# Kernel optimization log

Measured on AMD Instinct MI355X. Metric: run time of the kernel, lower is better.

Reference implementation:

```python
import jax, jax.numpy as jnp
import numpy as np

B = 64        # num_groups
G = 32        # group_size
D = 2000      # output dim (counts per bin/gene)
M = 16        # m_samples
E = 16        # noise_dim
DIN = 256
LAM = 1.0
TRUST = 0.25
SMOOTH = 1e-8
IPF_ITERS = 60
EPS = 1e-12


def _arch(x, noise, W, b):
    # simple linear architecture: concat(x, noise) @ W + b
    return jnp.concatenate([x, noise], axis=-1) @ W + b


def _loss(x, target, W, b, noise_loss):
    # replicate each row m times (unsqueeze(1).expand(...).reshape == repeat)
    x_rep = jnp.repeat(x, M, axis=0)                      # [n*M, DIN]
    pred = _arch(x_rep, noise_loss, W, b)                 # [n*M, D] (no act_fn in loss path)
    pred = pred.reshape(B, G, M, D).sum(axis=1)           # [B, M, D]
    term_conf = jnp.linalg.norm(pred - target[:, None, :], axis=2).mean(axis=1)  # [B]
    sq = jnp.sum(pred * pred, axis=2)                     # [B, M]
    inn = jnp.einsum('bmd,bnd->bmn', pred, pred)          # [B, M, M]
    sqd = jnp.clip(sq[:, :, None] + sq[:, None, :] - 2.0 * inn, 1e-6)
    d = jnp.sqrt(sqd)
    mask = 1.0 - jnp.eye(M, dtype=d.dtype)
    mean_pd = jnp.sum(d * mask, axis=(1, 2)) / (M * (M - 1))
    return jnp.mean(term_conf - (LAM / 2.0) * mean_pd)


def _ipf(x_pred, C):
    # KL/I-projection with row anchoring (keep_rows=True, trust_clip=0.25)
    y = jnp.clip(x_pred, 0.0)
    C = jnp.clip(C.astype(y.dtype), 0.0)
    R = y.sum(axis=2)                                     # [B, G] anchor row totals
    col_zero = (y.sum(axis=1) <= 0) & (C > 0)
    y = y + SMOOTH * col_zero[:, None, :].astype(y.dtype)
    row_zero = (y.sum(axis=2) <= 0) & (R > 0)
    y = y + SMOOTH * row_zero[:, :, None].astype(y.dtype)

    def body(_, y):
        col = jnp.clip(y.sum(axis=1), EPS)
        y = y * jnp.clip(C / col, 1.0 - TRUST, 1.0 + TRUST)[:, None, :]
        row = jnp.clip(y.sum(axis=2), EPS)
        y = y * jnp.clip(R / row, 1.0 - TRUST, 1.0 + TRUST)[:, :, None]
        return y

    y = jax.lax.fori_loop(0, IPF_ITERS, body, y)
    col = jnp.clip(y.sum(axis=1), EPS)
    return y * (C / col)[:, None, :]


def _rank(v, descending):
    # rank along last axis via double argsort (0 = first picked)
    order = jnp.argsort(-v if descending else v, axis=-1)
    return jnp.argsort(order, axis=-1)


def _round_to_targets(x, target_bd):
    # exact integerization across G per (B, D); jit-safe full-G rank replaces dynamic-k topk+scatter
    x = jnp.clip(x, 0.0)
    xf = jnp.floor(x)
    y = xf.astype(jnp.int32)                              # [B, G, D]
    frac = x - xf
    need = target_bd - y.sum(axis=1)                      # [B, D]
    pos = jnp.clip(need, 0)
    q = pos // G
    y = y + q[:, None, :]
    r = pos - q * G
    rank = _rank(jnp.transpose(frac, (0, 2, 1)), descending=True)   # [B, D, G]
    add = (rank < r[:, :, None]).astype(jnp.int32)
    y = y + jnp.transpose(add, (0, 2, 1))
    # negative residuals: remove from smallest frac among y > 0
    need = target_bd - y.sum(axis=1)
    neg = jnp.clip(-need, 0)
    neg = jnp.minimum(neg, y.sum(axis=1))
    q = neg // G
    y_before = y
    y = jnp.clip(y - q[:, None, :], 0)
    removed = (y_before - y).sum(axis=1)
    r = neg - removed
    frac_m = jnp.where(y > 0, frac, jnp.inf)
    rank = _rank(jnp.transpose(frac_m, (0, 2, 1)), descending=False)
    rem = (rank < r[:, :, None]).astype(jnp.int32)
    y = jnp.clip(y - jnp.transpose(rem, (0, 2, 1)), 0)
    return y


def setup_inputs() -> dict:
    key = jax.random.key(0)
    ks = jax.random.split(key, 6)
    x = jax.random.normal(ks[0], (B * G, DIN), dtype=jnp.float32)
    target = jax.random.uniform(ks[1], (B, D), dtype=jnp.float32) * 100.0
    target_sum = jax.random.randint(ks[2], (B, D), 0, 200, dtype=jnp.int32)
    W = jax.random.normal(ks[3], (DIN + E, D), dtype=jnp.float32) * 0.02
    b = jnp.zeros((D,), dtype=jnp.float32)
    noise_loss = jax.random.normal(ks[4], (B * G * M, E), dtype=jnp.float32)
    noise_sample = jax.random.normal(ks[5], (B * G, E), dtype=jnp.float32)
    return {"x": x, "target": target, "target_sum": target_sum, "W": W, "b": b,
            "noise_loss": noise_loss, "noise_sample": noise_sample}


def reference(x, target, target_sum, W, b, noise_loss, noise_sample):
    loss = _loss(x, target, W, b, noise_loss)
    # conditional_sample pipeline (no-grad in original): softplus act (min_value==0)
    x_pred = jax.nn.softplus(_arch(x, noise_sample, W, b)).reshape(B, G, D)
    y_float = _ipf(x_pred, target_sum.astype(jnp.float32))
    y_int = _round_to_targets(y_float, target_sum.astype(jnp.int32))
    return loss, y_int.reshape(B * G, D)
```

## Files before the change

### kernel.cpp

```cpp
#include <hip/hip_runtime.h>
#include <math.h>

#define NB   64
#define NG   32
#define ND   2000
#define NM   16
#define NE   16
#define NDIN 256
#define NK   272
#define NWAVES 16

__device__ __forceinline__ float clampf(float v, float lo, float hi) {
    return fminf(fmaxf(v, lo), hi);
}

__device__ __forceinline__ float softplusf(float v) {
    return (v > 20.f) ? v : log1pf(expf(v));
}

__device__ __forceinline__ float readlane_f(float v, int lane) {
    return __int_as_float(__builtin_amdgcn_readlane(__float_as_int(v), lane));
}

__device__ __forceinline__ float wave_sum32(float v[NG], int lane) {
    {   const bool hi = (lane & 32) != 0;
        #pragma unroll
        for (int k = 0; k < 16; ++k) {
            float s = hi ? v[k] : v[k + 16];
            float r = __shfl_xor(s, 32);
            v[k] = (hi ? v[k + 16] : v[k]) + r;
        }
    }
    {   const bool hi = (lane & 16) != 0;
        #pragma unroll
        for (int k = 0; k < 8; ++k) {
            float s = hi ? v[k] : v[k + 8];
            float r = __shfl_xor(s, 16);
            v[k] = (hi ? v[k + 8] : v[k]) + r;
        }
    }
    {   const bool hi = (lane & 8) != 0;
        #pragma unroll
        for (int k = 0; k < 4; ++k) {
            float s = hi ? v[k] : v[k + 4];
            float r = __shfl_xor(s, 8);
            v[k] = (hi ? v[k + 4] : v[k]) + r;
        }
    }
    {   const bool hi = (lane & 4) != 0;
        #pragma unroll
        for (int k = 0; k < 2; ++k) {
            float s = hi ? v[k] : v[k + 2];
            float r = __shfl_xor(s, 4);
            v[k] = (hi ? v[k + 2] : v[k]) + r;
        }
    }
    {   const bool hi = (lane & 2) != 0;
        float s = hi ? v[0] : v[1];
        float r = __shfl_xor(s, 2);
        v[0] = (hi ? v[1] : v[0]) + r;
    }
    v[0] += __shfl_xor(v[0], 1);
    return v[0];
}


__device__ __forceinline__ void ipf_path(
        const float* __restrict__ xp, const int* __restrict__ tsum,
        float* __restrict__ out, float* smem, int b, int t) {
    const int lane = t & 63, w = t >> 6;
    const int d0 = t * 2;
    const bool valid = (d0 < ND);
    const int g_own = (lane >> 1) & 31;

    float* wred = smem;

    float y0r[2][NG];
    #pragma unroll
    for (int g = 0; g < NG; ++g) {
        float2 v = make_float2(0.f, 0.f);
        if (valid) v = *(const float2*)(xp + (size_t)(b * NG + g) * ND + d0);
        y0r[0][g] = fmaxf(v.x, 0.f);
        y0r[1][g] = fmaxf(v.y, 0.f);
    }
    float Cc[2] = {0.f, 0.f};
    if (valid) {
        const int2 ci = *(const int2*)(tsum + (size_t)b * ND + d0);
        Cc[0] = (float)ci.x; Cc[1] = (float)ci.y;
    }
    float Ac[2] = {1.f, 1.f};
    float Bown = 1.f;
    float Rown;

    {
        float v[NG];
        #pragma unroll
        for (int g = 0; g < NG; ++g)
            v[g] = y0r[0][g] + y0r[1][g];
        const float tot = wave_sum32(v, lane);
        if ((lane & 1) == 0) wred[w * NG + g_own] = tot;
        __syncthreads();
        float s = 0.f;
        #pragma unroll
        for (int w2 = 0; w2 < NWAVES; ++w2) s += wred[w2 * NG + g_own];
        Rown = s;
    }

    for (int q = 1; q <= 60; ++q) {
        float s0 = 0.f, s1 = 0.f;
        #pragma unroll
        for (int g = 0; g < NG; ++g) {
            const float bg = readlane_f(Bown, 2 * g);
            s0 += y0r[0][g] * bg; s1 += y0r[1][g] * bg;
        }
        Ac[0] *= clampf(Cc[0] / fmaxf(Ac[0] * s0, 1e-12f), 0.75f, 1.25f);
        Ac[1] *= clampf(Cc[1] / fmaxf(Ac[1] * s1, 1e-12f), 0.75f, 1.25f);
        float v[NG];
        #pragma unroll
        for (int g = 0; g < NG; ++g)
            v[g] = y0r[0][g] * Ac[0] + y0r[1][g] * Ac[1];
        const float tot = wave_sum32(v, lane);
        const int buf = (q & 1) * (NWAVES * NG);
        if ((lane & 1) == 0) wred[buf + w * NG + g_own] = tot;
        __syncthreads();
        float s = 0.f;
        #pragma unroll
        for (int w2 = 0; w2 < NWAVES; ++w2) s += wred[buf + w2 * NG + g_own];
        Bown *= clampf(Rown / fmaxf(Bown * s, 1e-12f), 0.75f, 1.25f);
    }

    if (!valid) return;

    unsigned pk[NG];
    #pragma unroll
    for (int g = 0; g < NG; ++g) pk[g] = 0u;

    #pragma unroll
    for (int j = 0; j < 2; ++j) {
        float fr[NG];
        int   yv[NG];
        float s = 0.f;
        #pragma unroll
        for (int g = 0; g < NG; ++g) {
            const float z = y0r[j][g] * Ac[j] * readlane_f(Bown, 2 * g);
            fr[g] = z;
            s += z;
        }
        const float F = Cc[j] / fmaxf(s, 1e-12f);
        int isum = 0;
        #pragma unroll
        for (int g = 0; g < NG; ++g) {
            const float y = fr[g] * F;
            const float fl = floorf(y);
            yv[g] = (int)fl;
            fr[g] = y - fl;
            isum += yv[g];
        }
        const int Ci = (int)Cc[j];
        const int need = Ci - isum;
        const int pos = max(need, 0);
        const int qq = pos >> 5;
        const int r = pos & 31;
        #pragma unroll
        for (int g = 0; g < NG; ++g) yv[g] += qq;
        #pragma unroll
        for (int g = 0; g < NG; ++g) {
            int rank = 0;
            #pragma unroll
            for (int h = 0; h < NG; ++h) {
                if (h == g) continue;
                rank += (h < g) ? (fr[h] >= fr[g] ? 1 : 0) : (fr[h] > fr[g] ? 1 : 0);
            }
            if (rank < r) yv[g] += 1;
        }
        int neg = max(-need, 0);
        neg = min(neg, isum);
        if (__builtin_expect(neg > 0, 0)) {
            const int q2 = neg >> 5;
            int removed = 0;
            #pragma unroll
            for (int g = 0; g < NG; ++g) {
                const int yb = yv[g];
                const int yn = max(yb - q2, 0);
                removed += yb - yn;
                yv[g] = yn;
            }
            const int r2 = neg - removed;
            if (r2 > 0) {
                const float INF = __builtin_inff();
                #pragma unroll
                for (int g = 0; g < NG; ++g) {
                    const float fg = (yv[g] > 0) ? fr[g] : INF;
                    int rank = 0;
                    #pragma unroll
                    for (int h = 0; h < NG; ++h) {
                        if (h == g) continue;
                        const float fh = (yv[h] > 0) ? fr[h] : INF;
                        rank += (h < g) ? (fh <= fg ? 1 : 0) : (fh < fg ? 1 : 0);
                    }
                    if (rank < r2) yv[g] = max(yv[g] - 1, 0);
                }
            }
        }
        #pragma unroll
        for (int g = 0; g < NG; ++g)
            pk[g] |= ((unsigned)yv[g]) << (8 * j);
    }
    #pragma unroll
    for (int g = 0; g < NG; ++g) {
        float* op = &out[1 + (size_t)(b * NG + g) * ND + d0];
        op[0] = (float)(pk[g] & 0xffu);
        op[1] = (float)((pk[g] >> 8) & 0xffu);
    }
}

__device__ __forceinline__ void loss_path(
        const float* __restrict__ x, const float* __restrict__ nl,
        const float* __restrict__ tgt, const float* __restrict__ W,
        const float* __restrict__ bias, float* __restrict__ res2,
        float* smem, int cx, int b, int tt) {
    const int half = cx & 1;
    float* xsl = smem;
    float* nsl = smem + 256;
    float* tgl = smem + 512 + half * 4284;
    float* pt  = tgl + 252;

    if (half == 0 && tt < 256) {
        const float* xb = x + (size_t)b * NG * NDIN;
        float s = 0.f;
        for (int g = 0; g < NG; ++g) s += xb[g * NDIN + tt];
        xsl[tt] = s;
        const float* nb = nl + (size_t)b * NG * (NM * NE);
        float s2 = 0.f;
        for (int g = 0; g < NG; ++g) s2 += nb[g * (NM * NE) + tt];
        nsl[tt] = s2;
    }

    int tm = 0, tn = 0;
    if (tt >= 16 && tt < 152) {
        int p = tt - 16;
        for (int m = 0; m < NM; ++m) {
            int c = NM - m;
            if (p < c) { tm = m; tn = m + p; break; }
            p -= c;
        }
    }
    __syncthreads();

    const int d = cx * 250 + tt;
    if (tt < 250) {
        tgl[tt] = tgt[b * ND + d];
        float xw = 0.f;
        #pragma unroll 8
        for (int k = 0; k < NDIN; ++k) xw += xsl[k] * W[(size_t)k * ND + d];
        float we[NE];
        #pragma unroll
        for (int e = 0; e < NE; ++e) we[e] = W[(size_t)(NDIN + e) * ND + d];
        const float base0 = xw + (float)NG * bias[d];
        #pragma unroll
        for (int m = 0; m < NM; ++m) {
            float pm = base0;
            #pragma unroll
            for (int e = 0; e < NE; ++e) pm += nsl[m * NE + e] * we[e];
            pt[m * 252 + tt] = pm;
        }
    }
    if (tt < 32) {
        pt[(tt >> 1) * 252 + 250 + (tt & 1)] = 0.f;
        if (tt < 2) tgl[250 + tt] = 0.f;
    }
    __syncthreads();

    float acc = 0.f;
    if (tt < 16) {
        const float4* pa  = (const float4*)&pt[tt * 252];
        const float4* tga = (const float4*)&tgl[0];
        for (int i = 0; i < 63; ++i) {
            float4 pv = pa[i], tv = tga[i];
            float e0 = pv.x - tv.x, e1 = pv.y - tv.y, e2 = pv.z - tv.z, e3 = pv.w - tv.w;
            acc += e0 * e0 + e1 * e1 + e2 * e2 + e3 * e3;
        }
    } else if (tt < 152) {
        const float4* pa = (const float4*)&pt[tm * 252];
        const float4* pb = (const float4*)&pt[tn * 252];
        for (int i = 0; i < 63; ++i) {
            float4 u = pa[i], v = pb[i];
            acc += u.x * v.x + u.y * v.y + u.z * v.z + u.w * v.w;
        }
    }
    if (tt < 152) res2[((size_t)b * 8 + cx) * 152 + tt] = acc;
}

extern "C" __global__ __launch_bounds__(1024)
__attribute__((amdgpu_waves_per_eu(4, 4)))
void mega(const float* __restrict__ x, const float* __restrict__ nl,
          const float* __restrict__ tgt, const float* __restrict__ W,
          const float* __restrict__ bias, const float* __restrict__ xp,
          const int* __restrict__ tsum, float* __restrict__ out,
          float* __restrict__ res2) {
    __shared__ float smem[9080];
    const int bid = blockIdx.x;
    const int t = threadIdx.x;
    if (bid < NB) {
        ipf_path(xp, tsum, out, smem, bid, t);
    } else {
        const int q = bid - NB;
        const int b = q >> 2;
        const int cx = ((q & 3) << 1) | (t >> 9);
        loss_path(x, nl, tgt, W, bias, res2, smem, cx, b, t & 511);
    }
}

extern "C" __global__ __launch_bounds__(64)
void k2b_combine(const float* __restrict__ res2, float* __restrict__ out) {
    const int b = blockIdx.x, t = threadIdx.x;
    __shared__ float res[152];
    for (int tau = t; tau < 152; tau += 64) {
        float s = 0.f;
        #pragma unroll
        for (int c = 0; c < 8; ++c) s += res2[((size_t)b * 8 + c) * 152 + tau];
        res[tau] = s;
    }
    __syncthreads();
    if (t == 0) {
        float conf = 0.f;
        for (int m = 0; m < NM; ++m) conf += sqrtf(res[m]);
        conf *= (1.f / NM);
        float pd = 0.f;
        for (int m = 0; m < NM; ++m) {
            const int offm = 16 + m * NM - m * (m - 1) / 2;
            const float sqm = res[offm];
            for (int n = m + 1; n < NM; ++n) {
                const int offn = 16 + n * NM - n * (n - 1) / 2;
                const float sqn = res[offn];
                const float inn = res[offm + (n - m)];
                pd += sqrtf(fmaxf(sqm + sqn - 2.f * inn, 1e-6f));
            }
        }
        pd = 2.f * pd / (float)(NM * (NM - 1));
        atomicAdd(out, (conf - 0.5f * pd) * (1.f / NB));
    }
}

extern "C" __global__ __launch_bounds__(256)
void k3_xpred(const float* __restrict__ x, const float* __restrict__ nsamp,
              const float* __restrict__ W, const float* __restrict__ bias,
              float* __restrict__ xp) {
    const int dx = blockIdx.x;
    const int rb = blockIdx.y;
    const int t  = threadIdx.x;
    __shared__ float xr[8][NK];
    #pragma unroll
    for (int r = 0; r < 8; ++r) {
        const int row = rb * 8 + r;
        xr[r][t] = x[(size_t)row * NDIN + t];
        if (t < NE) xr[r][NDIN + t] = nsamp[row * NE + t];
    }
    __syncthreads();
    if (t >= 250) return;
    const int d = dx * 1000 + 4 * t;
    float acc[8][4];
    #pragma unroll
    for (int r = 0; r < 8; ++r) {
        acc[r][0] = 0.f; acc[r][1] = 0.f; acc[r][2] = 0.f; acc[r][3] = 0.f;
    }
    for (int k = 0; k < NK; k += 4) {
        float4 w[4];
        #pragma unroll
        for (int kk = 0; kk < 4; ++kk) w[kk] = *(const float4*)&W[(size_t)(k + kk) * ND + d];
        #pragma unroll
        for (int r = 0; r < 8; ++r) {
            const float4 xv = *(const float4*)&xr[r][k];
            acc[r][0] += xv.x * w[0].x + xv.y * w[1].x + xv.z * w[2].x + xv.w * w[3].x;
            acc[r][1] += xv.x * w[0].y + xv.y * w[1].y + xv.z * w[2].y + xv.w * w[3].y;
            acc[r][2] += xv.x * w[0].z + xv.y * w[1].z + xv.z * w[2].z + xv.w * w[3].z;
            acc[r][3] += xv.x * w[0].w + xv.y * w[1].w + xv.z * w[2].w + xv.w * w[3].w;
        }
    }
    const float4 bv = *(const float4*)&bias[d];
    #pragma unroll
    for (int r = 0; r < 8; ++r) {
        float4 o;
        o.x = softplusf(acc[r][0] + bv.x);
        o.y = softplusf(acc[r][1] + bv.y);
        o.z = softplusf(acc[r][2] + bv.z);
        o.w = softplusf(acc[r][3] + bv.w);
        *(float4*)&xp[(size_t)(rb * 8 + r) * ND + d] = o;
    }
}

extern "C" void kernel_launch(void* const* d_in, const int* in_sizes, int n_in,
                              void* d_out, int out_size, void* d_ws, size_t ws_size,
                              hipStream_t stream) {
    const float* x     = (const float*)d_in[0];
    const float* tgt   = (const float*)d_in[1];
    const int*   tsum  = (const int*)d_in[2];
    const float* W     = (const float*)d_in[3];
    const float* bias  = (const float*)d_in[4];
    const float* nl    = (const float*)d_in[5];
    const float* nsamp = (const float*)d_in[6];
    float* out = (float*)d_out;
    float* xp  = (float*)d_ws;

    (void)in_sizes; (void)n_in; (void)out_size; (void)ws_size;

    const size_t XPB = (size_t)2048 * 2000 * 4;
    float* res2 = (float*)((char*)d_ws + XPB);

    hipMemsetAsync(d_out, 0, sizeof(float), stream);

    hipLaunchKernelGGL(k3_xpred, dim3(2, 256), dim3(256), 0, stream,
                       x, nsamp, W, bias, xp);
    hipLaunchKernelGGL(mega, dim3(NB + 256), dim3(1024), 0, stream,
                       x, nl, tgt, W, bias, xp, tsum, out, res2);
    hipLaunchKernelGGL(k2b_combine, dim3(NB), dim3(64), 0, stream, res2, out);
}
```

Measured before the change: 336.0 us.

## Stage IPF matrix in LDS with transposed xpred layout instead of registers

The xpred kernel now writes its output transposed ([b][d][g]), so each IPF thread reads its 32 group values for its two columns as contiguous float4s. Instead of keeping 64 floats per thread in registers, the IPF path stages them in a large dynamic LDS buffer (about 160 KB) with a rotation swizzle. Columns beyond what fits in LDS re-read global memory every iteration. The waves_per_eu attribute is removed to relieve register pressure. The cost is LDS traffic on every iteration, and the larger shared allocation may limit how many blocks, including loss-path blocks, can share a CU.

```diff
diff --git a/kernel.cpp b/kernel.cpp
--- a/kernel.cpp
+++ b/kernel.cpp
@@ -10,6 +10,10 @@
 #define NK   272
 #define NWAVES 16
 
+#define LDST 608
+#define YB   4096
+#define SMEM_BYTES (YB + 1216 * 128)
+
 __device__ __forceinline__ float clampf(float v, float lo, float hi) {
     return fminf(fmaxf(v, lo), hi);
 }
@@ -64,25 +68,21 @@
     return v[0];
 }
 
-
 __device__ __forceinline__ void ipf_path(
-        const float* __restrict__ xp, const int* __restrict__ tsum,
-        float* __restrict__ out, float* smem, int b, int t) {
+        const float* __restrict__ xpT, const int* __restrict__ tsum,
+        float* __restrict__ out, char* smem, int b, int t) {
     const int lane = t & 63, w = t >> 6;
     const int d0 = t * 2;
     const bool valid = (d0 < ND);
+    const bool lcls  = (t < LDST);
     const int g_own = (lane >> 1) & 31;
-
-    float* wred = smem;
-
-    float y0r[2][NG];
-    #pragma unroll
-    for (int g = 0; g < NG; ++g) {
-        float2 v = make_float2(0.f, 0.f);
-        if (valid) v = *(const float2*)(xp + (size_t)(b * NG + g) * ND + d0);
-        y0r[0][g] = fmaxf(v.x, 0.f);
-        y0r[1][g] = fmaxf(v.y, 0.f);
-    }
+    const int rot = t & 7;
+
+    float* wred = (float*)smem;
+    char* base0 = smem + YB + (size_t)d0 * 128;
+    char* base1 = base0 + 128;
+    const float4* gp = (const float4*)(xpT + ((size_t)b * ND + d0) * NG);
+
     float Cc[2] = {0.f, 0.f};
     if (valid) {
         const int2 ci = *(const int2*)(tsum + (size_t)b * ND + d0);
@@ -94,9 +94,25 @@
 
     {
         float v[NG];
-        #pragma unroll
-        for (int g = 0; g < NG; ++g)
-            v[g] = y0r[0][g] + y0r[1][g];
+        if (valid) {
+            #pragma unroll
+            for (int k = 0; k < 8; ++k) {
+                const float4 a = gp[k];
+                const float4 c = gp[8 + k];
+                v[4*k+0] = a.x + c.x;
+                v[4*k+1] = a.y + c.y;
+                v[4*k+2] = a.z + c.z;
+                v[4*k+3] = a.w + c.w;
+                if (lcls) {
+                    const int ro = 16 * ((k + rot) & 7);
+                    *(float4*)(base0 + ro) = a;
+                    *(float4*)(base1 + ro) = c;
+                }
+            }
+        } else {
+            #pragma unroll
+            for (int g = 0; g < NG; ++g) v[g] = 0.f;
+        }
         const float tot = wave_sum32(v, lane);
         if ((lane & 1) == 0) wred[w * NG + g_own] = tot;
         __syncthreads();
@@ -108,17 +124,61 @@
 
     for (int q = 1; q <= 60; ++q) {
         float s0 = 0.f, s1 = 0.f;
-        #pragma unroll
-        for (int g = 0; g < NG; ++g) {
-            const float bg = readlane_f(Bown, 2 * g);
-            s0 += y0r[0][g] * bg; s1 += y0r[1][g] * bg;
+        if (lcls) {
+            #pragma unroll
+            for (int k = 0; k < 8; ++k) {
+                const int ro = 16 * ((k + rot) & 7);
+                const float4 a = *(const float4*)(base0 + ro);
+                const float4 c = *(const float4*)(base1 + ro);
+                float bg;
+                bg = readlane_f(Bown, 8*k+0); s0 += a.x * bg; s1 += c.x * bg;
+                bg = readlane_f(Bown, 8*k+2); s0 += a.y * bg; s1 += c.y * bg;
+                bg = readlane_f(Bown, 8*k+4); s0 += a.z * bg; s1 += c.z * bg;
+                bg = readlane_f(Bown, 8*k+6); s0 += a.w * bg; s1 += c.w * bg;
+            }
+        } else if (valid) {
+            #pragma unroll
+            for (int k = 0; k < 8; ++k) {
+                const float4 a = gp[k];
+                const float4 c = gp[8 + k];
+                float bg;
+                bg = readlane_f(Bown, 8*k+0); s0 += a.x * bg; s1 += c.x * bg;
+                bg = readlane_f(Bown, 8*k+2); s0 += a.y * bg; s1 += c.y * bg;
+                bg = readlane_f(Bown, 8*k+4); s0 += a.z * bg; s1 += c.z * bg;
+                bg = readlane_f(Bown, 8*k+6); s0 += a.w * bg; s1 += c.w * bg;
+            }
         }
         Ac[0] *= clampf(Cc[0] / fmaxf(Ac[0] * s0, 1e-12f), 0.75f, 1.25f);
         Ac[1] *= clampf(Cc[1] / fmaxf(Ac[1] * s1, 1e-12f), 0.75f, 1.25f);
+
+        asm volatile("" ::: "memory");
+
         float v[NG];
-        #pragma unroll
-        for (int g = 0; g < NG; ++g)
-            v[g] = y0r[0][g] * Ac[0] + y0r[1][g] * Ac[1];
+        if (lcls) {
+            #pragma unroll
+            for (int k = 0; k < 8; ++k) {
+                const int ro = 16 * ((k + rot) & 7);
+                const float4 a = *(const float4*)(base0 + ro);
+                const float4 c = *(const float4*)(base1 + ro);
+                v[4*k+0] = a.x * Ac[0] + c.x * Ac[1];
+                v[4*k+1] = a.y * Ac[0] + c.y * Ac[1];
+                v[4*k+2] = a.z * Ac[0] + c.z * Ac[1];
+                v[4*k+3] = a.w * Ac[0] + c.w * Ac[1];
+            }
+        } else if (valid) {
+            #pragma unroll
+            for (int k = 0; k < 8; ++k) {
+                const float4 a = gp[k];
+                const float4 c = gp[8 + k];
+                v[4*k+0] = a.x * Ac[0] + c.x * Ac[1];
+                v[4*k+1] = a.y * Ac[0] + c.y * Ac[1];
+                v[4*k+2] = a.z * Ac[0] + c.z * Ac[1];
+                v[4*k+3] = a.w * Ac[0] + c.w * Ac[1];
+            }
+        } else {
+            #pragma unroll
+            for (int g = 0; g < NG; ++g) v[g] = 0.f;
+        }
         const float tot = wave_sum32(v, lane);
         const int buf = (q & 1) * (NWAVES * NG);
         if ((lane & 1) == 0) wred[buf + w * NG + g_own] = tot;
@@ -131,20 +191,33 @@
 
     if (!valid) return;
 
-    unsigned pk[NG];
-    #pragma unroll
-    for (int g = 0; g < NG; ++g) pk[g] = 0u;
-
     #pragma unroll
     for (int j = 0; j < 2; ++j) {
         float fr[NG];
         int   yv[NG];
         float s = 0.f;
-        #pragma unroll
-        for (int g = 0; g < NG; ++g) {
-            const float z = y0r[j][g] * Ac[j] * readlane_f(Bown, 2 * g);
-            fr[g] = z;
-            s += z;
+        const char* basej = (j == 0) ? base0 : base1;
+        if (lcls) {
+            #pragma unroll
+            for (int k = 0; k < 8; ++k) {
+                const int ro = 16 * ((k + rot) & 7);
+                const float4 a = *(const float4*)(basej + ro);
+                float z;
+                z = a.x * Ac[j] * readlane_f(Bown, 8*k+0); fr[4*k+0] = z; s += z;
+                z = a.y * Ac[j] * readlane_f(Bown, 8*k+2); fr[4*k+1] = z; s += z;
+                z = a.z * Ac[j] * readlane_f(Bown, 8*k+4); fr[4*k+2] = z; s += z;
+                z = a.w * Ac[j] * readlane_f(Bown, 8*k+6); fr[4*k+3] = z; s += z;
+            }
+        } else {
+            #pragma unroll
+            for (int k = 0; k < 8; ++k) {
+                const float4 a = gp[j * 8 + k];
+                float z;
+                z = a.x * Ac[j] * readlane_f(Bown, 8*k+0); fr[4*k+0] = z; s += z;
+                z = a.y * Ac[j] * readlane_f(Bown, 8*k+2); fr[4*k+1] = z; s += z;
+                z = a.z * Ac[j] * readlane_f(Bown, 8*k+4); fr[4*k+2] = z; s += z;
+                z = a.w * Ac[j] * readlane_f(Bown, 8*k+6); fr[4*k+3] = z; s += z;
+            }
         }
         const float F = Cc[j] / fmaxf(s, 1e-12f);
         int isum = 0;
@@ -204,13 +277,7 @@
         }
         #pragma unroll
         for (int g = 0; g < NG; ++g)
-            pk[g] |= ((unsigned)yv[g]) << (8 * j);
-    }
-    #pragma unroll
-    for (int g = 0; g < NG; ++g) {
-        float* op = &out[1 + (size_t)(b * NG + g) * ND + d0];
-        op[0] = (float)(pk[g] & 0xffu);
-        op[1] = (float)((pk[g] >> 8) & 0xffu);
+            out[1 + (size_t)(b * NG + g) * ND + d0 + j] = (float)yv[g];
     }
 }
 
@@ -292,22 +359,21 @@
 }
 
 extern "C" __global__ __launch_bounds__(1024)
-__attribute__((amdgpu_waves_per_eu(4, 4)))
 void mega(const float* __restrict__ x, const float* __restrict__ nl,
           const float* __restrict__ tgt, const float* __restrict__ W,
-          const float* __restrict__ bias, const float* __restrict__ xp,
+          const float* __restrict__ bias, const float* __restrict__ xpT,
           const int* __restrict__ tsum, float* __restrict__ out,
           float* __restrict__ res2) {
-    __shared__ float smem[9080];
+    extern __shared__ char smem[];
     const int bid = blockIdx.x;
     const int t = threadIdx.x;
     if (bid < NB) {
-        ipf_path(xp, tsum, out, smem, bid, t);
+        ipf_path(xpT, tsum, out, smem, bid, t);
     } else {
         const int q = bid - NB;
         const int b = q >> 2;
         const int cx = ((q & 3) << 1) | (t >> 9);
-        loss_path(x, nl, tgt, W, bias, res2, smem, cx, b, t & 511);
+        loss_path(x, nl, tgt, W, bias, res2, (float*)smem, cx, b, t & 511);
     }
 }
 
@@ -345,7 +411,7 @@
 extern "C" __global__ __launch_bounds__(256)
 void k3_xpred(const float* __restrict__ x, const float* __restrict__ nsamp,
               const float* __restrict__ W, const float* __restrict__ bias,
-              float* __restrict__ xp) {
+              float* __restrict__ xpT) {
     const int dx = blockIdx.x;
     const int rb = blockIdx.y;
     const int t  = threadIdx.x;
@@ -378,14 +444,23 @@
         }
     }
     const float4 bv = *(const float4*)&bias[d];
+    const float bvv[4] = {bv.x, bv.y, bv.z, bv.w};
+    const int b2 = rb >> 2;
+    const int g0 = (rb & 3) * 8;
     #pragma unroll
-    for (int r = 0; r < 8; ++r) {
-        float4 o;
-        o.x = softplusf(acc[r][0] + bv.x);
-        o.y = softplusf(acc[r][1] + bv.y);
-        o.z = softplusf(acc[r][2] + bv.z);
-        o.w = softplusf(acc[r][3] + bv.w);
-        *(float4*)&xp[(size_t)(rb * 8 + r) * ND + d] = o;
+    for (int dd = 0; dd < 4; ++dd) {
+        float* op = xpT + ((size_t)b2 * ND + (d + dd)) * NG + g0;
+        float4 lo, hi;
+        lo.x = softplusf(acc[0][dd] + bvv[dd]);
+        lo.y = softplusf(acc[1][dd] + bvv[dd]);
+        lo.z = softplusf(acc[2][dd] + bvv[dd]);
+        lo.w = softplusf(acc[3][dd] + bvv[dd]);
+        hi.x = softplusf(acc[4][dd] + bvv[dd]);
+        hi.y = softplusf(acc[5][dd] + bvv[dd]);
+        hi.z = softplusf(acc[6][dd] + bvv[dd]);
+        hi.w = softplusf(acc[7][dd] + bvv[dd]);
+        *(float4*)op       = lo;
+        *(float4*)(op + 4) = hi;
     }
 }
 
@@ -400,18 +475,26 @@
     const float* nl    = (const float*)d_in[5];
     const float* nsamp = (const float*)d_in[6];
     float* out = (float*)d_out;
-    float* xp  = (float*)d_ws;
+    float* xpT = (float*)d_ws;
 
     (void)in_sizes; (void)n_in; (void)out_size; (void)ws_size;
 
     const size_t XPB = (size_t)2048 * 2000 * 4;
     float* res2 = (float*)((char*)d_ws + XPB);
 
+    static int s_attr_done = 0;
+    if (!s_attr_done) {
+        hipFuncSetAttribute(reinterpret_cast<const void*>(mega),
+                            hipFuncAttributeMaxDynamicSharedMemorySize,
+                            SMEM_BYTES);
+        s_attr_done = 1;
+    }
+
     hipMemsetAsync(d_out, 0, sizeof(float), stream);
 
     hipLaunchKernelGGL(k3_xpred, dim3(2, 256), dim3(256), 0, stream,
-                       x, nsamp, W, bias, xp);
-    hipLaunchKernelGGL(mega, dim3(NB + 256), dim3(1024), 0, stream,
-                       x, nl, tgt, W, bias, xp, tsum, out, res2);
+                       x, nsamp, W, bias, xpT);
+    hipLaunchKernelGGL(mega, dim3(NB + 256), dim3(1024), SMEM_BYTES, stream,
+                       x, nl, tgt, W, bias, xpT, tsum, out, res2);
     hipLaunchKernelGGL(k2b_combine, dim3(NB), dim3(64), 0, stream, res2, out);
 }
```

Result: slower. 587.8 us (+75.0%).
